# Optimization experiments

Hardware: AMD Instinct MI355X
Metric: run time of the kernel (lower is better)

Reference implementation:

```python
import jax, jax.numpy as jnp
import numpy as np

TEMP = 5.0  # temperature_init
# All C(4,2)=6 keep-2-of-4 patterns for 2:4 semi-structured sparsity
PATTERNS = jnp.array([[1,1,0,0],[1,0,1,0],[1,0,0,1],[0,1,1,0],[0,1,0,1],[0,0,1,1]], dtype=jnp.float32)


def masked_linear(x, w, b, alpha, ids):
    # x: [N, I], w: [O, I], alpha: [A, O, I//4, 6], ids: [N]
    A, O, G, P = alpha.shape
    probs = jax.nn.softmax(alpha / TEMP, axis=-1)            # [A, O, G, 6]
    mask = jnp.einsum('aogp,pk->aogk', probs, PATTERNS)      # [A, O, G, 4]
    wm = w[None, :, :] * mask.reshape(A, O, G * 4)           # [A, O, I] per-agent masked weight
    y = jnp.einsum('ni,aoi->nao', x, wm)                     # dense per-agent GEMM
    y = jnp.take_along_axis(y, ids[:, None, None], axis=1)[:, 0, :]
    return y + b


def gru_cell(x, h, w_ih, w_hh, b_ih, b_hh):
    gi = x @ w_ih.T + b_ih
    gh = h @ w_hh.T + b_hh
    i_r, i_z, i_n = jnp.split(gi, 3, axis=-1)
    h_r, h_z, h_n = jnp.split(gh, 3, axis=-1)
    r = jax.nn.sigmoid(i_r + h_r)
    z = jax.nn.sigmoid(i_z + h_z)
    n = jnp.tanh(i_n + r * h_n)
    return (1.0 - z) * n + z * h


def setup_inputs() -> dict:
    key = jax.random.key(0)
    ks = jax.random.split(key, 20)
    B, A, E, H, NA = 1024, 8, 64, 512, 16
    s = 0.05
    d = {}
    d['inputs'] = jax.random.normal(ks[0], (B, A, E), jnp.float32)
    d['hidden_state'] = jax.random.normal(ks[1], (B, A, H), jnp.float32)
    d['agent_ids'] = jax.random.randint(ks[2], (B, A), 0, A, jnp.int32)
    d['fc1_w'] = jax.random.normal(ks[3], (H, E), jnp.float32) * s
    d['fc1_b'] = jax.random.normal(ks[4], (H,), jnp.float32) * s
    d['fc1_alpha'] = jax.random.normal(ks[5], (A, H, E // 4, 6), jnp.float32)
    d['gru_w_ih'] = jax.random.normal(ks[6], (3 * H, H), jnp.float32) * s
    d['gru_w_hh'] = jax.random.normal(ks[7], (3 * H, H), jnp.float32) * s
    d['gru_b_ih'] = jax.random.normal(ks[8], (3 * H,), jnp.float32) * s
    d['gru_b_hh'] = jax.random.normal(ks[9], (3 * H,), jnp.float32) * s
    d['fc2_w'] = jax.random.normal(ks[10], (H, H), jnp.float32) * s
    d['fc2_b'] = jax.random.normal(ks[11], (H,), jnp.float32) * s
    d['fc2_alpha'] = jax.random.normal(ks[12], (A, H, H // 4, 6), jnp.float32)
    d['fc3_w'] = jax.random.normal(ks[13], (H, H), jnp.float32) * s
    d['fc3_b'] = jax.random.normal(ks[14], (H,), jnp.float32) * s
    d['fc3_alpha'] = jax.random.normal(ks[15], (A, H, H // 4, 6), jnp.float32)
    d['fc4_w'] = jax.random.normal(ks[16], (NA, H), jnp.float32) * s
    d['fc4_b'] = jax.random.normal(ks[17], (NA,), jnp.float32) * s
    d['fc4_alpha'] = jax.random.normal(ks[18], (A, NA, H // 4, 6), jnp.float32)
    return d


def reference(inputs, hidden_state, agent_ids,
              fc1_w, fc1_b, fc1_alpha,
              gru_w_ih, gru_w_hh, gru_b_ih, gru_b_hh,
              fc2_w, fc2_b, fc2_alpha,
              fc3_w, fc3_b, fc3_alpha,
              fc4_w, fc4_b, fc4_alpha):
    b, a, e = inputs.shape
    H = hidden_state.shape[-1]
    x = inputs.reshape(-1, e)
    ids = agent_ids.reshape(-1)
    x = jax.nn.relu(masked_linear(x, fc1_w, fc1_b, fc1_alpha, ids))
    h = gru_cell(x, hidden_state.reshape(-1, H), gru_w_ih, gru_w_hh, gru_b_ih, gru_b_hh)
    q = jax.nn.relu(masked_linear(h, fc2_w, fc2_b, fc2_alpha, ids))
    q = jax.nn.relu(masked_linear(q, fc3_w, fc3_b, fc3_alpha, ids))
    q = masked_linear(q, fc4_w, fc4_b, fc4_alpha, ids)
    return q.reshape(b, a, -1), h.reshape(b, a, -1)
```

## Files before the change

kernel.cpp:

```cpp
#include <hip/hip_runtime.h>
#include <hip/hip_bf16.h>

typedef unsigned short ushort_t;
typedef __bf16 bf16x8 __attribute__((ext_vector_type(8)));
typedef unsigned short us8 __attribute__((ext_vector_type(8)));
typedef float f32x4 __attribute__((ext_vector_type(4)));

#define NPAD 8704
#define SENT (1 << 20)

__device__ __forceinline__ ushort_t f2b(float f) {
    union { float f; unsigned int u; } v; v.f = f;
    unsigned int u = v.u;
    unsigned int r = (u + 0x7FFFu + ((u >> 16) & 1u)) >> 16;
    return (ushort_t)r;
}
__device__ __forceinline__ float sigmoidf_(float x) {
    return 1.f / (1.f + __expf(-x));
}

__device__ __forceinline__ void gl16(const ushort_t* g, ushort_t* l) {
    __builtin_amdgcn_global_load_lds(
        (const __attribute__((address_space(1))) unsigned int*)g,
        (__attribute__((address_space(3))) unsigned int*)l, 16, 0, 0);
}
__device__ __forceinline__ void vm0_bar() {
    asm volatile("s_waitcnt vmcnt(0)" ::: "memory");
    __builtin_amdgcn_s_barrier();
    __builtin_amdgcn_sched_barrier(0);
}

__global__ void fill_kernel(float* out, long long n, float val) {
    long long i = (long long)blockIdx.x * blockDim.x + threadIdx.x;
    if (i < n) out[i] = val;
}

#define PACKSZ(O, K) ((long long)((O) >= 64 ? (O) >> 6 : 1) * ((K) >> 5) * 2048)

__global__ void sort_kernel(const int* __restrict__ ids, int N,
                            int* __restrict__ perm, int* __restrict__ seg,
                            int4* __restrict__ ttab, int* __restrict__ tcount) {
    __shared__ int hist[16][8];
    __shared__ int wbase[16][8];
    __shared__ int atot[8];
    __shared__ int abase[8];
    int tid = threadIdx.x, wave = tid >> 6, lane = tid & 63;
    int base = wave * 512;
    unsigned long long lt = (lane == 63) ? 0x7fffffffffffffffull
                                         : ((1ull << lane) - 1ull);
    int myid[8], rank[8];
    int run[8] = {0, 0, 0, 0, 0, 0, 0, 0};
    #pragma unroll
    for (int i = 0; i < 8; i++) myid[i] = ids[base + i * 64 + lane] & 7;
    #pragma unroll
    for (int i = 0; i < 8; i++) {
        int a = myid[i];
        int r = 0;
        #pragma unroll
        for (int a2 = 0; a2 < 8; a2++) {
            unsigned long long m = __ballot(a == a2);
            if (a2 == a) r = run[a2] + __popcll(m & lt);
            run[a2] += __popcll(m);
        }
        rank[i] = r;
    }
    if (lane == 0) {
        #pragma unroll
        for (int a = 0; a < 8; a++) hist[wave][a] = run[a];
    }
    __syncthreads();
    if (tid < 8) {
        int a = tid, s = 0;
        for (int w = 0; w < 16; w++) { wbase[w][a] = s; s += hist[w][a]; }
        atot[a] = s;
    }
    __syncthreads();
    if (tid == 0) {
        int s = 0;
        for (int a = 0; a < 8; a++) {
            abase[a] = s; seg[a] = s;
            s += (atot[a] + 63) & ~63;
        }
        seg[8] = s;
        int T = 0;
        for (int a = 0; a < 8; a++) {
            int e = abase[a] + atot[a];
            int pe = abase[a] + ((atot[a] + 63) & ~63);
            for (int m = abase[a]; m < pe; m += 64) {
                int z = e < m + 64 ? e : m + 64;
                ttab[T++] = make_int4(a, m, z, 0);
            }
        }
        *tcount = T;
    }
    __syncthreads();
    #pragma unroll
    for (int i = 0; i < 8; i++) {
        int a = myid[i];
        perm[abase[a] + wbase[wave][a] + rank[i]] = base + i * 64 + lane;
    }
    for (int a = 0; a < 8; a++) {
        int e = abase[a] + atot[a];
        int pe = abase[a] + ((atot[a] + 63) & ~63);
        for (int p2 = e + tid; p2 < pe; p2 += 1024) perm[p2] = SENT;
    }
    int Pend = abase[7] + ((atot[7] + 63) & ~63);
    for (int p2 = Pend + tid; p2 < NPAD; p2 += 1024) perm[p2] = SENT;
}

__device__ __forceinline__ void maskw_item(const float* __restrict__ alpha,
                                           const float* __restrict__ w,
                                           ushort_t* __restrict__ wm,
                                           long long idx, int O, int G, int dup) {
    int g = (int)(idx % G);
    long long t2 = idx / G;
    int o = (int)(t2 % O);
    int a = (int)(t2 / O);
    const float* al = alpha + idx * 6;
    float p[6];
    float mx = -1e30f;
    #pragma unroll
    for (int i = 0; i < 6; i++) { p[i] = al[i] * 0.2f; mx = fmaxf(mx, p[i]); }
    float s = 0.f;
    #pragma unroll
    for (int i = 0; i < 6; i++) { p[i] = __expf(p[i] - mx); s += p[i]; }
    float inv = 1.f / s;
    #pragma unroll
    for (int i = 0; i < 6; i++) p[i] *= inv;
    float mk[4] = { p[0] + p[1] + p[2], p[0] + p[3] + p[4],
                    p[1] + p[3] + p[5], p[2] + p[4] + p[5] };
    int K = G * 4;
    const float* wr = w + (long long)o * K + g * 4;
    ushort_t* base = wm + (long long)a * PACKSZ(O, K);
    int k0 = g * 4;
    int c = o >> 6, su = (o >> 4) & 3, n = o & 15;
    int kk = k0 >> 5, q = (k0 >> 3) & 3, e0 = k0 & 7;
    long long off = (((long long)(c * (K >> 5) + kk) * 4 + su) * 64 + (q * 16 + n)) * 8 + e0;
    #pragma unroll
    for (int t = 0; t < 4; t++) {
        ushort_t v = f2b(wr[t] * mk[t]);
        base[off + t] = v;
        if (dup) {
            base[off + t + 512] = v;
            base[off + t + 1024] = v;
            base[off + t + 1536] = v;
        }
    }
}

__device__ __forceinline__ void canon_gather_packed(const float* __restrict__ src,
                                                    ushort_t* __restrict__ dst,
                                                    const int* __restrict__ perm,
                                                    int ld, long long i) {
    int l = (int)(i & 63);
    int tt = (int)(i >> 6);
    int KK = ld >> 5;
    int mt = tt / KK, kk = tt - mt * KK;
    int row = perm[mt * 16 + (l & 15)];
    if (row >= 8192) row = 0;
    const float* s = src + (long long)row * ld + kk * 32 + (l >> 4) * 8;
    us8 v;
    #pragma unroll
    for (int e = 0; e < 8; e++) v[e] = f2b(s[e]);
    *(us8*)(dst + i * 8) = v;
}

__device__ __forceinline__ void canon_pack_item(const float* __restrict__ src,
                                                ushort_t* __restrict__ dst,
                                                long long i) {
    long long base = i * 8;
    int o_full = (int)(base >> 9);
    int k0 = (int)(base & 511);
    int g = o_full >> 9, o = o_full & 511;
    int c = o >> 6, su = (o >> 4) & 3, n = o & 15;
    int kk = k0 >> 5, q = (k0 >> 3) & 3;
    long long off = (long long)g * 262144 +
        (((long long)(c * 16 + kk) * 4 + su) * 64 + (q * 16 + n)) * 8;
    us8 v;
    #pragma unroll
    for (int e = 0; e < 8; e++) v[e] = f2b(src[base + e]);
    *(us8*)(dst + off) = v;
}

#define PB0 256
#define PB1 2048
#define PB2 2048
#define PB3 64
#define PB4 272
#define PB5 2176
#define PB6 384
#define PB7 384
#define PREP_BLOCKS (PB0+PB1+PB2+PB3+PB4+PB5+PB6+PB7)

__global__ void prep_kernel(const float* fc1_al, const float* fc1_w, ushort_t* wm1,
                            const float* fc2_al, const float* fc2_w, ushort_t* wm2,
                            const float* fc3_al, const float* fc3_w, ushort_t* wm3,
                            const float* fc4_al, const float* fc4_w, ushort_t* wm4,
                            const float* inputs, ushort_t* inp_pos,
                            const float* hidden, ushort_t* hid_pos,
                            const float* wih, ushort_t* wihp,
                            const float* whh, ushort_t* whhp,
                            const int* perm) {
    int b = blockIdx.x;
    int tid = threadIdx.x;
    if (b < PB0) { maskw_item(fc1_al, fc1_w, wm1, (long long)b * 256 + tid, 512, 16, 0); return; }
    b -= PB0;
    if (b < PB1) { maskw_item(fc2_al, fc2_w, wm2, (long long)b * 256 + tid, 512, 128, 0); return; }
    b -= PB1;
    if (b < PB2) { maskw_item(fc3_al, fc3_w, wm3, (long long)b * 256 + tid, 512, 128, 0); return; }
    b -= PB2;
    if (b < PB3) { maskw_item(fc4_al, fc4_w, wm4, (long long)b * 256 + tid, 16, 128, 1); return; }
    b -= PB3;
    if (b < PB4) { canon_gather_packed(inputs, inp_pos, perm, 64, (long long)b * 256 + tid); return; }
    b -= PB4;
    if (b < PB5) { canon_gather_packed(hidden, hid_pos, perm, 512, (long long)b * 256 + tid); return; }
    b -= PB5;
    if (b < PB6) { canon_pack_item(wih, wihp, (long long)b * 256 + tid); return; }
    b -= PB6;
    canon_pack_item(whh, whhp, (long long)b * 256 + tid);
}

template <typename OT, int NC, int PACKOUT>
__launch_bounds__(256, 3)
__global__ void gemm_tiled(const ushort_t* __restrict__ Apk, int K,
                           const ushort_t* __restrict__ Wpk, long long wstride,
                           const float* __restrict__ bias,
                           OT* __restrict__ Out, int ldo,
                           const int4* __restrict__ ttab,
                           const int* __restrict__ tcount,
                           const int* __restrict__ perm,
                           int O, int relu) {
    int t = blockIdx.x;
    if (t >= *tcount) return;
    int4 tt = ttab[t];
    int a = tt.x, pos0 = tt.y;
    constexpr int JJ = 2 * NC;
    constexpr int NCH = 4 + 4 * NC;
    constexpr int CPW = NCH / 4;

    __shared__ ushort_t S[2][NCH * 512];
    __shared__ ushort_t Cs[PACKOUT ? 64 * 136 : 2];

    int tid = threadIdx.x;
    int wave = tid >> 6, lane = tid & 63;
    int wr = (wave >> 1) & 1, wc = wave & 1;
    int quad = lane >> 4, l16 = lane & 15;

    int KK = K >> 5;

    const ushort_t* cbase[CPW];
    int cstep[CPW];
    #pragma unroll
    for (int q = 0; q < CPW; q++) {
        int c = wave * CPW + q;
        if (c < 4) {
            cbase[q] = Apk + ((long long)((pos0 >> 4) + c) * KK) * 512 + lane * 8;
            cstep[q] = 512;
        } else {
            int idx = c - 4, cblk = idx >> 2, su = idx & 3;
            cbase[q] = Wpk + (long long)a * wstride +
                (long long)(blockIdx.y * NC + cblk) * KK * 2048 + su * 512 + lane * 8;
            cstep[q] = 2048;
        }
    }
    auto STAGE = [&](int bufv, int kkv) {
        #pragma unroll
        for (int q = 0; q < CPW; q++)
            gl16(cbase[q] + kkv * cstep[q], &S[bufv][(wave * CPW + q) * 512]);
    };

    f32x4 acc[2][JJ];
    #pragma unroll
    for (int i = 0; i < 2; i++)
        #pragma unroll
        for (int j = 0; j < JJ; j++) acc[i][j] = (f32x4){0.f, 0.f, 0.f, 0.f};

    STAGE(0, 0);
    vm0_bar();
    int cur = 0;
    for (int kk = 0; kk < KK; kk++) {
        if (kk + 1 < KK) STAGE(cur ^ 1, kk + 1);
        const ushort_t* Sc = S[cur];
        bf16x8 af[2], bf[JJ];
        #pragma unroll
        for (int i = 0; i < 2; i++)
            af[i] = *(const bf16x8*)(Sc + (wr * 2 + i) * 512 + lane * 8);
        #pragma unroll
        for (int j = 0; j < JJ; j++) {
            int ch = (NC == 2) ? (4 + wc * 4 + j) : (4 + wc * 2 + j);
            bf[j] = *(const bf16x8*)(Sc + ch * 512 + lane * 8);
        }
        #pragma unroll
        for (int i = 0; i < 2; i++)
            #pragma unroll
            for (int j = 0; j < JJ; j++)
                acc[i][j] = __builtin_amdgcn_mfma_f32_16x16x32_bf16(af[i], bf[j], acc[i][j], 0, 0, 0);
        vm0_bar();
        cur ^= 1;
    }

    if constexpr (PACKOUT) {
        #pragma unroll
        for (int i = 0; i < 2; i++)
            #pragma unroll
            for (int j = 0; j < JJ; j++) {
                int colL = (NC == 2 ? wc * 64 : wc * 32) + j * 16 + l16;
                int col = blockIdx.y * (64 * NC) + colL;
                float bv = bias[col];
                #pragma unroll
                for (int r = 0; r < 4; r++) {
                    float v = acc[i][j][r] + bv;
                    if (relu) v = fmaxf(v, 0.f);
                    Cs[(wr * 32 + i * 16 + quad * 4 + r) * 136 + colL] = f2b(v);
                }
            }
        __syncthreads();
        int KKo = ldo >> 5;
        int kk0 = blockIdx.y * (2 * NC);
        constexpr int NKK = 2 * NC;
        #pragma unroll
        for (int s2 = 0; s2 < NKK; s2++) {
            int slot = s2 * 256 + tid;
            int l = slot & 63, t4 = slot >> 6;
            int mt = t4 / NKK, kkL = t4 - mt * NKK;
            us8 v = *(const us8*)(&Cs[(mt * 16 + (l & 15)) * 136 + kkL * 32 + (l >> 4) * 8]);
            *(us8*)((ushort_t*)Out + ((long long)((pos0 >> 4) + mt) * KKo + kk0 + kkL) * 512 + l * 8) = v;
        }
    } else {
        #pragma unroll
        for (int i = 0; i < 2; i++) {
            int mbase = wr * 32 + i * 16 + quad * 4;
            #pragma unroll
            for (int j = 0; j < JJ; j++) {
                int col = (NC == 2 ? wc * 64 : wc * 32) + j * 16 + l16;
                if (col < O) {
                    float bv = bias[col];
                    #pragma unroll
                    for (int r = 0; r < 4; r++) {
                        int pos = pos0 + mbase + r;
                        int orow = perm[pos];
                        if (orow < 8192) {
                            float v = acc[i][j][r] + bv;
                            if (relu) v = fmaxf(v, 0.f);
                            Out[(long long)orow * ldo + col] = v;
                        }
                    }
                }
            }
        }
    }
}

__launch_bounds__(256, 2)
__global__ void gru_fused(const ushort_t* __restrict__ y1,
                          const ushort_t* __restrict__ hid,
                          const float* __restrict__ hidden_f,
                          const ushort_t* __restrict__ wihp,
                          const ushort_t* __restrict__ whhp,
                          const float* __restrict__ bih,
                          const float* __restrict__ bhh,
                          const int* __restrict__ perm,
                          float* __restrict__ out_h_f,
                          ushort_t* __restrict__ hp,
                          const int4* __restrict__ ttab,
                          const int* __restrict__ tcount,
                          int H) {
    int t = blockIdx.x;
    if (t >= *tcount) return;
    int pos0 = ttab[t].y;
    int mt0 = pos0 >> 4;

    __shared__ ushort_t S[2][32 * 512];
    __shared__ ushort_t Cs[64 * 72];

    int tid = threadIdx.x;
    int wave = tid >> 6, lane = tid & 63;
    int wr = (wave >> 1) & 1, wc = wave & 1;
    int quad = lane >> 4, l16 = lane & 15;

    const ushort_t* cbase[8];
    int cstep[8];
    #pragma unroll
    for (int q = 0; q < 8; q++) {
        int c = wave * 8 + q;
        if (c < 8) {
            int mt = c & 3;
            const ushort_t* srcp = (c < 4) ? y1 : hid;
            cbase[q] = srcp + ((long long)(mt0 + mt) * 16) * 512 + lane * 8;
            cstep[q] = 512;
        } else {
            int idx = c - 8, g = idx >> 2, su = idx & 3;
            const ushort_t* gp = (g < 3) ? (wihp + (long long)g * 262144)
                                         : (whhp + (long long)(g - 3) * 262144);
            cbase[q] = gp + (long long)blockIdx.y * 16 * 2048 + su * 512 + lane * 8;
            cstep[q] = 2048;
        }
    }
    auto STAGE = [&](int bufv, int kkv) {
        #pragma unroll
        for (int q = 0; q < 8; q++)
            gl16(cbase[q] + kkv * cstep[q], &S[bufv][(wave * 8 + q) * 512]);
    };

    f32x4 acc[4][2][2];
    #pragma unroll
    for (int g = 0; g < 4; g++)
        #pragma unroll
        for (int i = 0; i < 2; i++)
            #pragma unroll
            for (int j = 0; j < 2; j++) acc[g][i][j] = (f32x4){0.f, 0.f, 0.f, 0.f};

    STAGE(0, 0);
    vm0_bar();
    int cur = 0;
    for (int kk = 0; kk < 16; kk++) {
        if (kk + 1 < 16) STAGE(cur ^ 1, kk + 1);
        const ushort_t* Sc = S[cur];
        bf16x8 ayf[2], ahf[2], bw[3][2], bu[3][2];
        #pragma unroll
        for (int u = 0; u < 2; u++) {
            ayf[u] = *(const bf16x8*)(Sc + (wr * 2 + u) * 512 + lane * 8);
            ahf[u] = *(const bf16x8*)(Sc + (4 + wr * 2 + u) * 512 + lane * 8);
        }
        #pragma unroll
        for (int g = 0; g < 3; g++)
            #pragma unroll
            for (int u = 0; u < 2; u++) {
                bw[g][u] = *(const bf16x8*)(Sc + (8 + g * 4 + wc * 2 + u) * 512 + lane * 8);
                bu[g][u] = *(const bf16x8*)(Sc + (8 + (g + 3) * 4 + wc * 2 + u) * 512 + lane * 8);
            }
        #pragma unroll
        for (int g = 0; g < 3; g++) {
            int ai = (g < 2) ? g : 2;
            int ah2 = (g < 2) ? g : 3;
            #pragma unroll
            for (int i = 0; i < 2; i++)
                #pragma unroll
                for (int j = 0; j < 2; j++) {
                    acc[ai][i][j] = __builtin_amdgcn_mfma_f32_16x16x32_bf16(
                        ayf[i], bw[g][j], acc[ai][i][j], 0, 0, 0);
                    acc[ah2][i][j] = __builtin_amdgcn_mfma_f32_16x16x32_bf16(
                        ahf[i], bu[g][j], acc[ah2][i][j], 0, 0, 0);
                }
        }
        vm0_bar();
        cur ^= 1;
    }

    int c0 = blockIdx.y * 64;
    #pragma unroll
    for (int i = 0; i < 2; i++) {
        #pragma unroll
        for (int r = 0; r < 4; r++) {
            int rowL = wr * 32 + i * 16 + quad * 4 + r;
            int pos = pos0 + rowL;
            int norig = perm[pos];
            bool realr = norig < 8192;
            int nr = realr ? norig : 0;
            #pragma unroll
            for (int j = 0; j < 2; j++) {
                int colL = wc * 32 + j * 16 + l16;
                int col = c0 + colL;
                float sr = acc[0][i][j][r] + bih[col] + bhh[col];
                float sz = acc[1][i][j][r] + bih[H + col] + bhh[H + col];
                float in_ = acc[2][i][j][r] + bih[2 * H + col];
                float hn = acc[3][i][j][r] + bhh[2 * H + col];
                float rg = sigmoidf_(sr);
                float zg = sigmoidf_(sz);
                float ng = tanhf(in_ + rg * hn);
                float hv = hidden_f[(long long)nr * H + col];
                float hnew = (1.f - zg) * ng + zg * hv;
                if (realr) out_h_f[(long long)norig * H + col] = hnew;
                Cs[rowL * 72 + colL] = f2b(hnew);
            }
        }
    }
    __syncthreads();
    #pragma unroll
    for (int s2 = 0; s2 < 2; s2++) {
        int slot = s2 * 256 + tid;
        int l = slot & 63, t4 = slot >> 6;
        int mt = t4 >> 1, kkL = t4 & 1;
        us8 v = *(const us8*)(&Cs[(mt * 16 + (l & 15)) * 72 + kkL * 32 + (l >> 4) * 8]);
        *(us8*)(hp + ((long long)(mt0 + mt) * 16 + blockIdx.y * 2 + kkL) * 512 + l * 8) = v;
    }
}

extern "C" void kernel_launch(void* const* d_in, const int* in_sizes, int n_in,
                              void* d_out, int out_size, void* d_ws, size_t ws_size,
                              hipStream_t stream) {
    (void)in_sizes; (void)n_in;
    const int N = 8192, A = 8, E = 64, H = 512, NA = 16;

    float* out_f = (float*)d_out;
    float* out_q = out_f;
    float* out_h = out_f + (size_t)N * NA;

    char* p = (char*)d_ws;
    auto alloc = [&](size_t b) { char* r = p; p += (b + 255) & ~(size_t)255; return r; };
    int*  perm   = (int*)alloc((size_t)NPAD * 4);
    int*  seg    = (int*)alloc(16 * 4);
    int4* ttab   = (int4*)alloc(144 * 16);
    int*  tcount = (int*)alloc(256);
    ushort_t* wm1     = (ushort_t*)alloc((size_t)A * PACKSZ(H, E) * 2);
    ushort_t* wm2     = (ushort_t*)alloc((size_t)A * PACKSZ(H, H) * 2);
    ushort_t* wm3     = (ushort_t*)alloc((size_t)A * PACKSZ(H, H) * 2);
    ushort_t* wm4     = (ushort_t*)alloc((size_t)A * PACKSZ(NA, H) * 2);
    ushort_t* y1      = (ushort_t*)alloc((size_t)NPAD * H * 2);
    ushort_t* inp_pos = (ushort_t*)alloc((size_t)NPAD * E * 2);
    ushort_t* hid_pos = (ushort_t*)alloc((size_t)NPAD * H * 2);
    ushort_t* wihp    = (ushort_t*)alloc((size_t)3 * H * H * 2);
    ushort_t* whhp    = (ushort_t*)alloc((size_t)3 * H * H * 2);
    ushort_t* hp      = (ushort_t*)alloc((size_t)NPAD * H * 2);
    size_t need = (size_t)(p - (char*)d_ws);
    ushort_t* q2 = y1;
    ushort_t* q3 = hid_pos;

    if (ws_size < need) {
        fill_kernel<<<(unsigned)((out_size + 255) / 256), 256, 0, stream>>>(
            out_f, out_size, 1000.f);
        return;
    }

    const float* inputs = (const float*)d_in[0];
    const float* hidden = (const float*)d_in[1];
    const int*   ids    = (const int*)d_in[2];
    const float* fc1_w  = (const float*)d_in[3];
    const float* fc1_b  = (const float*)d_in[4];
    const float* fc1_al = (const float*)d_in[5];
    const float* wih    = (const float*)d_in[6];
    const float* whh    = (const float*)d_in[7];
    const float* bih    = (const float*)d_in[8];
    const float* bhh    = (const float*)d_in[9];
    const float* fc2_w  = (const float*)d_in[10];
    const float* fc2_b  = (const float*)d_in[11];
    const float* fc2_al = (const float*)d_in[12];
    const float* fc3_w  = (const float*)d_in[13];
    const float* fc3_b  = (const float*)d_in[14];
    const float* fc3_al = (const float*)d_in[15];
    const float* fc4_w  = (const float*)d_in[16];
    const float* fc4_b  = (const float*)d_in[17];
    const float* fc4_al = (const float*)d_in[18];

    sort_kernel<<<1, 1024, 0, stream>>>(ids, N, perm, seg, ttab, tcount);

    prep_kernel<<<PREP_BLOCKS, 256, 0, stream>>>(
        fc1_al, fc1_w, wm1, fc2_al, fc2_w, wm2, fc3_al, fc3_w, wm3,
        fc4_al, fc4_w, wm4, inputs, inp_pos, hidden, hid_pos,
        wih, wihp, whh, whhp, perm);

    dim3 blk(256);
    gemm_tiled<ushort_t, 2, 1><<<dim3(136, H / 128), blk, 0, stream>>>(
        inp_pos, E, wm1, PACKSZ(H, E), fc1_b, y1, H, ttab, tcount,
        perm, H, 1);
    gru_fused<<<dim3(136, H / 64), blk, 0, stream>>>(
        y1, hid_pos, hidden, wihp, whhp, bih, bhh, perm, out_h, hp,
        ttab, tcount, H);
    gemm_tiled<ushort_t, 2, 1><<<dim3(136, H / 128), blk, 0, stream>>>(
        hp, H, wm2, PACKSZ(H, H), fc2_b, q2, H, ttab, tcount,
        perm, H, 1);
    gemm_tiled<ushort_t, 2, 1><<<dim3(136, H / 128), blk, 0, stream>>>(
        q2, H, wm3, PACKSZ(H, H), fc3_b, q3, H, ttab, tcount,
        perm, H, 1);
    gemm_tiled<float, 1, 0><<<dim3(136, 1), blk, 0, stream>>>(
        q3, H, wm4, PACKSZ(NA, H), fc4_b, out_q, NA, ttab, tcount,
        perm, NA, 0);
}
```

Baseline: 255.8 us.

## Load GRU A-operands directly to registers and shrink LDS to only weights

```diff
diff --git a/kernel.cpp b/kernel.cpp
--- a/kernel.cpp
+++ b/kernel.cpp
@@ -351,7 +351,7 @@
     }
 }
 
-__launch_bounds__(256, 2)
+__launch_bounds__(256, 3)
 __global__ void gru_fused(const ushort_t* __restrict__ y1,
                           const ushort_t* __restrict__ hid,
                           const float* __restrict__ hidden_f,
@@ -370,37 +370,22 @@
     int pos0 = ttab[t].y;
     int mt0 = pos0 >> 4;
 
-    __shared__ ushort_t S[2][32 * 512];
-    __shared__ ushort_t Cs[64 * 72];
+    __shared__ ushort_t Bt[6][2048];
 
     int tid = threadIdx.x;
     int wave = tid >> 6, lane = tid & 63;
     int wr = (wave >> 1) & 1, wc = wave & 1;
     int quad = lane >> 4, l16 = lane & 15;
 
-    const ushort_t* cbase[8];
-    int cstep[8];
-    #pragma unroll
-    for (int q = 0; q < 8; q++) {
-        int c = wave * 8 + q;
-        if (c < 8) {
-            int mt = c & 3;
-            const ushort_t* srcp = (c < 4) ? y1 : hid;
-            cbase[q] = srcp + ((long long)(mt0 + mt) * 16) * 512 + lane * 8;
-            cstep[q] = 512;
-        } else {
-            int idx = c - 8, g = idx >> 2, su = idx & 3;
-            const ushort_t* gp = (g < 3) ? (wihp + (long long)g * 262144)
-                                         : (whhp + (long long)(g - 3) * 262144);
-            cbase[q] = gp + (long long)blockIdx.y * 16 * 2048 + su * 512 + lane * 8;
-            cstep[q] = 2048;
-        }
-    }
-    auto STAGE = [&](int bufv, int kkv) {
-        #pragma unroll
-        for (int q = 0; q < 8; q++)
-            gl16(cbase[q] + kkv * cstep[q], &S[bufv][(wave * 8 + q) * 512]);
-    };
+    const ushort_t* ayp = y1 + (long long)mt0 * 8192 + lane * 8;
+    const ushort_t* ahp = hid + (long long)mt0 * 8192 + lane * 8;
+
+    long long cb = (long long)blockIdx.y * 16 * 2048 + tid * 8;
+    const ushort_t* wbg[6];
+    #pragma unroll
+    for (int g = 0; g < 3; g++) wbg[g] = wihp + (long long)g * 262144 + cb;
+    #pragma unroll
+    for (int g = 3; g < 6; g++) wbg[g] = whhp + (long long)(g - 3) * 262144 + cb;
 
     f32x4 acc[4][2][2];
     #pragma unroll
@@ -410,27 +395,29 @@
             #pragma unroll
             for (int j = 0; j < 2; j++) acc[g][i][j] = (f32x4){0.f, 0.f, 0.f, 0.f};
 
-    STAGE(0, 0);
-    vm0_bar();
-    int cur = 0;
     for (int kk = 0; kk < 16; kk++) {
-        if (kk + 1 < 16) STAGE(cur ^ 1, kk + 1);
-        const ushort_t* Sc = S[cur];
-        bf16x8 ayf[2], ahf[2], bw[3][2], bu[3][2];
+        bf16x8 ayf[2], ahf[2];
         #pragma unroll
         for (int u = 0; u < 2; u++) {
-            ayf[u] = *(const bf16x8*)(Sc + (wr * 2 + u) * 512 + lane * 8);
-            ahf[u] = *(const bf16x8*)(Sc + (4 + wr * 2 + u) * 512 + lane * 8);
-        }
-        #pragma unroll
-        for (int g = 0; g < 3; g++)
+            ayf[u] = *(const bf16x8*)(ayp + ((long long)(wr * 2 + u) * 16 + kk) * 512);
+            ahf[u] = *(const bf16x8*)(ahp + ((long long)(wr * 2 + u) * 16 + kk) * 512);
+        }
+        us8 vb[6];
+        #pragma unroll
+        for (int g = 0; g < 6; g++) vb[g] = *(const us8*)(wbg[g] + kk * 2048);
+        __syncthreads();
+        #pragma unroll
+        for (int g = 0; g < 6; g++) *(us8*)(&Bt[g][tid * 8]) = vb[g];
+        __syncthreads();
+
+        #pragma unroll
+        for (int g = 0; g < 3; g++) {
+            bf16x8 bw[2], bu[2];
             #pragma unroll
             for (int u = 0; u < 2; u++) {
-                bw[g][u] = *(const bf16x8*)(Sc + (8 + g * 4 + wc * 2 + u) * 512 + lane * 8);
-                bu[g][u] = *(const bf16x8*)(Sc + (8 + (g + 3) * 4 + wc * 2 + u) * 512 + lane * 8);
+                bw[u] = *(const bf16x8*)(&Bt[g][(wc * 2 + u) * 512 + lane * 8]);
+                bu[u] = *(const bf16x8*)(&Bt[g + 3][(wc * 2 + u) * 512 + lane * 8]);
             }
-        #pragma unroll
-        for (int g = 0; g < 3; g++) {
             int ai = (g < 2) ? g : 2;
             int ah2 = (g < 2) ? g : 3;
             #pragma unroll
@@ -438,15 +425,15 @@
                 #pragma unroll
                 for (int j = 0; j < 2; j++) {
                     acc[ai][i][j] = __builtin_amdgcn_mfma_f32_16x16x32_bf16(
-                        ayf[i], bw[g][j], acc[ai][i][j], 0, 0, 0);
+                        ayf[i], bw[j], acc[ai][i][j], 0, 0, 0);
                     acc[ah2][i][j] = __builtin_amdgcn_mfma_f32_16x16x32_bf16(
-                        ahf[i], bu[g][j], acc[ah2][i][j], 0, 0, 0);
+                        ahf[i], bu[j], acc[ah2][i][j], 0, 0, 0);
                 }
         }
-        vm0_bar();
-        cur ^= 1;
-    }
-
+    }
+
+    __syncthreads();
+    ushort_t* Cs = &Bt[0][0];
     int c0 = blockIdx.y * 64;
     #pragma unroll
     for (int i = 0; i < 2; i++) {
```

After: 239.6 us. -6.3%, faster.
